# Optimization experiments

Measured on AMD Instinct MI355X. Metric: run time of the kernel, lower is better.

Reference implementation:

```python
import jax, jax.numpy as jnp
import numpy as np
import math

B, S, D, H = 2, 2048, 2048, 16
HD = D // H  # 128


def setup_inputs() -> dict:
    key = jax.random.key(0)
    ks = jax.random.split(key, 6)
    x = jax.random.normal(ks[0], (B, S, D), dtype=jnp.float32)
    scale = 1.0 / math.sqrt(D)
    wq = jax.random.normal(ks[1], (D, D), dtype=jnp.float32) * scale
    wk = jax.random.normal(ks[2], (D, D), dtype=jnp.float32) * scale
    wv = jax.random.normal(ks[3], (D, D), dtype=jnp.float32) * scale
    wo = jax.random.normal(ks[4], (D, D), dtype=jnp.float32) * scale
    # rotary frequencies: freqs_cis[t, j] = exp(i * t / theta^(2j/HD))
    theta = 10000.0
    inv = 1.0 / (theta ** (jnp.arange(0, HD, 2, dtype=jnp.float32) / HD))  # [HD//2]
    ang = jnp.arange(S, dtype=jnp.float32)[:, None] * inv[None, :]  # [S, HD//2]
    freqs_cos = jnp.cos(ang)
    freqs_sin = jnp.sin(ang)
    # causal additive mask
    mask = jnp.where(jnp.tril(jnp.ones((S, S), dtype=bool)), 0.0, -1e9)
    mask = mask[None, None, :, :].astype(jnp.float32)
    return {"x": x, "wq": wq, "wk": wk, "wv": wv, "wo": wo,
            "freqs_cos": freqs_cos, "freqs_sin": freqs_sin, "mask": mask}


def _rope(t, cos, sin):
    # t: [B, S, H, HD]; cos/sin: [S, HD//2]
    b, s, h, d = t.shape
    t2 = t.reshape(b, s, h, d // 2, 2)
    re, im = t2[..., 0], t2[..., 1]
    c = cos[None, :, None, :]
    sn = sin[None, :, None, :]
    out_re = re * c - im * sn
    out_im = re * sn + im * c
    return jnp.stack([out_re, out_im], axis=-1).reshape(b, s, h, d)


def reference(x, wq, wk, wv, wo, freqs_cos, freqs_sin, mask):
    b, s, _ = x.shape
    xq = (x @ wq.T).reshape(b, s, H, HD)
    xk = (x @ wk.T).reshape(b, s, H, HD)
    xv = (x @ wv.T).reshape(b, s, H, HD)
    xq = _rope(xq, freqs_cos, freqs_sin)
    xk = _rope(xk, freqs_cos, freqs_sin)
    # [B, H, S, HD]
    q = xq.transpose(0, 2, 1, 3)
    k = xk.transpose(0, 2, 1, 3)
    v = xv.transpose(0, 2, 1, 3)
    scores = jnp.einsum("bhqd,bhkd->bhqk", q, k) / math.sqrt(HD)
    scores = scores + mask
    probs = jax.nn.softmax(scores.astype(jnp.float32), axis=-1).astype(q.dtype)
    out = jnp.einsum("bhqk,bhkd->bhqd", probs, v)
    out = out.transpose(0, 2, 1, 3).reshape(b, s, -1)
    return out @ wo.T
```

## Files before the change

kernel.cpp:

```cpp
#include <hip/hip_runtime.h>
#include <math.h>

#define BATCH 2
#define SEQ 2048
#define DMODEL 2048
#define NH 16
#define HD 128

typedef __bf16 bf16x8 __attribute__((ext_vector_type(8)));
typedef __bf16 bf16x4 __attribute__((ext_vector_type(4)));
typedef float f32x4 __attribute__((ext_vector_type(4)));
typedef float f32x16 __attribute__((ext_vector_type(16)));

#define GLL16(dst, src)                                                          \
  __builtin_amdgcn_global_load_lds(                                              \
      (const __attribute__((address_space(1))) void*)(src),                      \
      (__attribute__((address_space(3))) void*)(dst), 16, 0, 0)

__global__ __launch_bounds__(256) void split_fp32(const float* __restrict__ src,
                                                  __bf16* __restrict__ hi,
                                                  __bf16* __restrict__ lo) {
  const size_t i = (size_t)blockIdx.x * 256 + threadIdx.x;
  const float4 v = ((const float4*)src)[i];
  bf16x4 h, L;
  h[0] = (__bf16)v.x; h[1] = (__bf16)v.y; h[2] = (__bf16)v.z; h[3] = (__bf16)v.w;
  L[0] = (__bf16)(v.x - (float)h[0]);
  L[1] = (__bf16)(v.y - (float)h[1]);
  L[2] = (__bf16)(v.z - (float)h[2]);
  L[3] = (__bf16)(v.w - (float)h[3]);
  ((bf16x4*)hi)[i] = h;
  ((bf16x4*)lo)[i] = L;
}

template <int EMIT>
__global__ __launch_bounds__(256) void gemm_bs(const __bf16* __restrict__ Ah,
                                               const __bf16* __restrict__ Al,
                                               const __bf16* __restrict__ Bh,
                                               const __bf16* __restrict__ Bl,
                                               void* __restrict__ Cout,
                                               int M, int N, int K) {
  __shared__ __bf16 sAh[4096], sAl[4096], sBh[4096], sBl[4096];
  const int tid = threadIdx.x;
  const int l = tid & 63;
  const int w = tid >> 6;
  const int lg = l >> 4, lm = l & 15;
  const int wr = w >> 1, wc = w & 1;
  const int m0 = blockIdx.y * 128, n0 = blockIdx.x * 128;

  const int sr = l >> 2;
  const int sc8 = (l & 3) * 8;
  const size_t rowA0 = (size_t)(m0 + 32 * w + sr);
  const size_t rowB0 = (size_t)(n0 + 32 * w + sr);

  f32x4 acc[4][4];
#pragma unroll
  for (int i = 0; i < 4; ++i)
#pragma unroll
    for (int j = 0; j < 4; ++j) { f32x4 z = {0.f, 0.f, 0.f, 0.f}; acc[i][j] = z; }

  for (int k0 = 0; k0 < K; k0 += 32) {
    __syncthreads();
    GLL16(sAh + 1024 * w,       Ah + rowA0 * K + k0 + sc8);
    GLL16(sAh + 1024 * w + 512, Ah + (rowA0 + 16) * K + k0 + sc8);
    GLL16(sAl + 1024 * w,       Al + rowA0 * K + k0 + sc8);
    GLL16(sAl + 1024 * w + 512, Al + (rowA0 + 16) * K + k0 + sc8);
    GLL16(sBh + 1024 * w,       Bh + rowB0 * K + k0 + sc8);
    GLL16(sBh + 1024 * w + 512, Bh + (rowB0 + 16) * K + k0 + sc8);
    GLL16(sBl + 1024 * w,       Bl + rowB0 * K + k0 + sc8);
    GLL16(sBl + 1024 * w + 512, Bl + (rowB0 + 16) * K + k0 + sc8);
    __syncthreads();

    bf16x8 fah[4], fal[4], fbh[4], fbl[4];
#pragma unroll
    for (int i = 0; i < 4; ++i) {
      const int ra = (wr * 64 + 16 * i + lm) * 32 + lg * 8;
      fah[i] = *(const bf16x8*)(sAh + ra);
      fal[i] = *(const bf16x8*)(sAl + ra);
      const int rb = (wc * 64 + 16 * i + lm) * 32 + lg * 8;
      fbh[i] = *(const bf16x8*)(sBh + rb);
      fbl[i] = *(const bf16x8*)(sBl + rb);
    }
#pragma unroll
    for (int i = 0; i < 4; ++i)
#pragma unroll
      for (int j = 0; j < 4; ++j) {
        acc[i][j] = __builtin_amdgcn_mfma_f32_16x16x32_bf16(fah[i], fbh[j], acc[i][j], 0, 0, 0);
        acc[i][j] = __builtin_amdgcn_mfma_f32_16x16x32_bf16(fah[i], fbl[j], acc[i][j], 0, 0, 0);
        acc[i][j] = __builtin_amdgcn_mfma_f32_16x16x32_bf16(fal[i], fbh[j], acc[i][j], 0, 0, 0);
      }
  }

#pragma unroll
  for (int i = 0; i < 4; ++i)
#pragma unroll
    for (int j = 0; j < 4; ++j)
#pragma unroll
      for (int r = 0; r < 4; ++r) {
        const size_t row = (size_t)(m0 + wr * 64 + 16 * i + lg * 4 + r);
        const size_t col = (size_t)(n0 + wc * 64 + 16 * j + lm);
        if (EMIT == 0) ((float*)Cout)[row * N + col] = acc[i][j][r];
        else           ((__bf16*)Cout)[row * N + col] = (__bf16)acc[i][j][r];
      }
}

__global__ __launch_bounds__(256) void rope_bf16(__bf16* __restrict__ t,
                                                 const float* __restrict__ cosp,
                                                 const float* __restrict__ sinp,
                                                 float scale) {
  const size_t i4 = (size_t)blockIdx.x * 256 + threadIdx.x;
  const size_t e = i4 * 4;
  const int srow = (int)((e >> 11) & 2047);
  const int p = (int)(e & 127) >> 1;
  bf16x4 vv = *(bf16x4*)(t + e);
  const float c0 = cosp[srow * 64 + p],     s0 = sinp[srow * 64 + p];
  const float c1 = cosp[srow * 64 + p + 1], s1 = sinp[srow * 64 + p + 1];
  const float re0 = (float)vv[0], im0 = (float)vv[1];
  const float re1 = (float)vv[2], im1 = (float)vv[3];
  bf16x4 o;
  o[0] = (__bf16)((re0 * c0 - im0 * s0) * scale);
  o[1] = (__bf16)((re0 * s0 + im0 * c0) * scale);
  o[2] = (__bf16)((re1 * c1 - im1 * s1) * scale);
  o[3] = (__bf16)((re1 * s1 + im1 * c1) * scale);
  *(bf16x4*)(t + e) = o;
}

static __device__ __forceinline__ unsigned pk2(float a, float b) {
  unsigned short x = __builtin_bit_cast(unsigned short, (__bf16)a);
  unsigned short y = __builtin_bit_cast(unsigned short, (__bf16)b);
  return ((unsigned)y << 16) | (unsigned)x;
}

__global__ __launch_bounds__(256) void attn_mfma2(const __bf16* __restrict__ q,
                                                  const __bf16* __restrict__ k,
                                                  const __bf16* __restrict__ v,
                                                  __bf16* __restrict__ oh,
                                                  __bf16* __restrict__ ol) {
  __shared__ __align__(16) char Ks[64 * 272];
  __shared__ __align__(16) char Vt[128 * 144];

  const int tid = threadIdx.x;
  const int l = tid & 63, w = tid >> 6;
  const int l31 = l & 31, hg = l >> 5;

  const int f = (int)blockIdx.x;
  const int X = f & 7, t = f >> 3;
  const int g = X * 4 + (t & 3);
  const int qt = 15 - (t >> 2);
  const int b = g >> 4, h = g & 15;
  const int q0 = qt * 128;
  const size_t bh = (size_t)b * SEQ * DMODEL + (size_t)h * HD;

  bf16x8 qf[8];
  {
    const __bf16* qr = q + bh + (size_t)(q0 + 32 * w + l31) * DMODEL;
#pragma unroll
    for (int ks = 0; ks < 8; ++ks) qf[ks] = *(const bf16x8*)(qr + ks * 16 + hg * 8);
  }

  f32x16 accO[4];
#pragma unroll
  for (int dt = 0; dt < 4; ++dt)
#pragma unroll
    for (int i = 0; i < 16; ++i) accO[dt][i] = 0.f;
  float m_own = -1e30f, l_own = 0.f;

  const int srT = tid >> 4;
  const int scT = tid & 15;
  const int nkt = 2 * qt + 2;
  const int qg_own = q0 + 32 * w + l31;
  const int qg_min = q0 + 32 * w;

  bf16x8 kst[4], vst[4];
#pragma unroll
  for (int rnd = 0; rnd < 4; ++rnd) {
    const int r = srT + 16 * rnd;
    const size_t ga = bh + (size_t)(r) * DMODEL + scT * 8;
    kst[rnd] = *(const bf16x8*)(k + ga);
    vst[rnd] = *(const bf16x8*)(v + ga);
  }

  for (int kt = 0; kt < nkt; ++kt) {
    const int k0 = kt * 64;
    __syncthreads();
#pragma unroll
    for (int rnd = 0; rnd < 4; ++rnd) {
      const int r = srT + 16 * rnd;
      *(bf16x8*)(Ks + r * 272 + ((scT * 16) ^ (((r >> 3) & 7) << 4))) = kst[rnd];
      const int swz = (scT & 7) << 4;
      const int cb = (2 * r) ^ swz;
#pragma unroll
      for (int e = 0; e < 8; ++e)
        *(__bf16*)(Vt + (scT * 8 + e) * 144 + cb) = vst[rnd][e];
    }
    __syncthreads();
    if (kt + 1 < nkt) {
#pragma unroll
      for (int rnd = 0; rnd < 4; ++rnd) {
        const int r = srT + 16 * rnd;
        const size_t ga = bh + (size_t)((kt + 1) * 64 + r) * DMODEL + scT * 8;
        kst[rnd] = *(const bf16x8*)(k + ga);
        vst[rnd] = *(const bf16x8*)(v + ga);
      }
    }
    if (k0 > qg_min + 31) continue;

    f32x16 sc[2];
#pragma unroll
    for (int mt = 0; mt < 2; ++mt)
#pragma unroll
      for (int i = 0; i < 16; ++i) sc[mt][i] = 0.f;
#pragma unroll
    for (int mt = 0; mt < 2; ++mt) {
      const int row = mt * 32 + l31;
      const char* kr = Ks + row * 272;
      const int sx = ((row >> 3) & 7) << 4;
#pragma unroll
      for (int ks = 0; ks < 8; ++ks) {
        bf16x8 kf = *(const bf16x8*)(kr + ((ks * 32 + hg * 16) ^ sx));
        sc[mt] = __builtin_amdgcn_mfma_f32_32x32x16_bf16(kf, qf[ks], sc[mt], 0, 0, 0);
      }
    }

    if (k0 + 63 > qg_min) {
#pragma unroll
      for (int mt = 0; mt < 2; ++mt)
#pragma unroll
        for (int ri = 0; ri < 16; ++ri) {
          const int kg = k0 + mt * 32 + (ri & 3) + 8 * (ri >> 2) + 4 * hg;
          if (kg > qg_own) sc[mt][ri] = -INFINITY;
        }
    }

    float tm = -INFINITY;
#pragma unroll
    for (int mt = 0; mt < 2; ++mt)
#pragma unroll
      for (int ri = 0; ri < 16; ++ri) tm = fmaxf(tm, sc[mt][ri]);
    tm = fmaxf(tm, __shfl_xor(tm, 32));

    if (__any(tm > m_own)) {
      const float mnew = fmaxf(m_own, tm);
      const float alpha = __expf(m_own - mnew);
      m_own = mnew;
      l_own *= alpha;
#pragma unroll
      for (int ri = 0; ri < 16; ++ri) {
        const float a = __shfl(alpha, (ri & 3) + 8 * (ri >> 2) + 4 * hg);
#pragma unroll
        for (int dt = 0; dt < 4; ++dt) accO[dt][ri] *= a;
      }
    }
    float rs = 0.f;
#pragma unroll
    for (int mt = 0; mt < 2; ++mt)
#pragma unroll
      for (int ri = 0; ri < 16; ++ri) {
        const float p = __expf(sc[mt][ri] - m_own);
        sc[mt][ri] = p;
        rs += p;
      }
    rs += __shfl_xor(rs, 32);
    l_own += rs;

#pragma unroll
    for (int kk = 0; kk < 4; ++kk) {
      const int mt = kk >> 1, J8 = (kk & 1) * 8;
      unsigned oL0 = pk2(sc[mt][J8 + 0], sc[mt][J8 + 1]);
      unsigned oL1 = pk2(sc[mt][J8 + 2], sc[mt][J8 + 3]);
      unsigned oH0 = pk2(sc[mt][J8 + 4], sc[mt][J8 + 5]);
      unsigned oH1 = pk2(sc[mt][J8 + 6], sc[mt][J8 + 7]);
      unsigned s0 = hg ? oL0 : oH0;
      unsigned s1 = hg ? oL1 : oH1;
      const unsigned r0 = (unsigned)__shfl_xor((int)s0, 32);
      const unsigned r1 = (unsigned)__shfl_xor((int)s1, 32);
      int4 fi;
      fi.x = (int)(hg ? r0 : oL0);
      fi.y = (int)(hg ? r1 : oL1);
      fi.z = (int)(hg ? oH0 : r0);
      fi.w = (int)(hg ? oH1 : r1);
      const bf16x8 pa = __builtin_bit_cast(bf16x8, fi);
      const int kb = (kk * 32 + hg * 16);
#pragma unroll
      for (int dt = 0; dt < 4; ++dt) {
        const int d = dt * 32 + l31;
        bf16x8 vf = *(const bf16x8*)(Vt + d * 144 + (kb ^ (((d >> 3) & 7) << 4)));
        accO[dt] = __builtin_amdgcn_mfma_f32_32x32x16_bf16(pa, vf, accO[dt], 0, 0, 0);
      }
    }
  }

  const float inv_own = 1.f / l_own;
#pragma unroll
  for (int ri = 0; ri < 16; ++ri) {
    const int row = (ri & 3) + 8 * (ri >> 2) + 4 * hg;
    const float il = __shfl(inv_own, row & 31);
    const size_t rbase = bh + (size_t)(q0 + 32 * w + row) * DMODEL;
#pragma unroll
    for (int dt = 0; dt < 4; ++dt) {
      const float val = accO[dt][ri] * il;
      const size_t idx = rbase + dt * 32 + l31;
      const __bf16 hv = (__bf16)val;
      oh[idx] = hv;
      ol[idx] = (__bf16)(val - (float)hv);
    }
  }
}

extern "C" void kernel_launch(void* const* d_in, const int* in_sizes, int n_in,
                              void* d_out, int out_size, void* d_ws, size_t ws_size,
                              hipStream_t stream) {
  const float* x  = (const float*)d_in[0];
  const float* wq = (const float*)d_in[1];
  const float* wk = (const float*)d_in[2];
  const float* wv = (const float*)d_in[3];
  const float* wo = (const float*)d_in[4];
  const float* fc = (const float*)d_in[5];
  const float* fs = (const float*)d_in[6];

  const size_t NTOK = (size_t)BATCH * SEQ;
  const size_t NE   = NTOK * DMODEL;

  char* wsb = (char*)d_ws;
  __bf16* xh = (__bf16*)wsb;
  __bf16* xl = xh + NE;
  __bf16* wh = (__bf16*)(wsb + 2 * NE * 2);
  __bf16* wl = wh + (size_t)DMODEL * DMODEL;
  __bf16* vb = (__bf16*)(wsb + 2 * NE * 2 + 2 * (size_t)DMODEL * DMODEL * 2);
  __bf16* oh = xh;
  __bf16* ol = xl;
  __bf16* qb = (__bf16*)d_out;
  __bf16* kb = qb + NE;

  const dim3 gg(DMODEL / 128, (unsigned)(NTOK / 128));
  const int sx = (int)(NE / 4 / 256);
  const int sw = DMODEL * DMODEL / 4 / 256;

  split_fp32<<<sx, 256, 0, stream>>>(x, xh, xl);

  split_fp32<<<sw, 256, 0, stream>>>(wq, wh, wl);
  gemm_bs<1><<<gg, 256, 0, stream>>>(xh, xl, wh, wl, qb, (int)NTOK, DMODEL, DMODEL);
  split_fp32<<<sw, 256, 0, stream>>>(wk, wh, wl);
  gemm_bs<1><<<gg, 256, 0, stream>>>(xh, xl, wh, wl, kb, (int)NTOK, DMODEL, DMODEL);
  split_fp32<<<sw, 256, 0, stream>>>(wv, wh, wl);
  gemm_bs<1><<<gg, 256, 0, stream>>>(xh, xl, wh, wl, vb, (int)NTOK, DMODEL, DMODEL);

  rope_bf16<<<sx, 256, 0, stream>>>(qb, fc, fs, 0.08838834764831845f);
  rope_bf16<<<sx, 256, 0, stream>>>(kb, fc, fs, 1.0f);

  attn_mfma2<<<dim3(512), 256, 0, stream>>>(qb, kb, vb, oh, ol);

  split_fp32<<<sw, 256, 0, stream>>>(wo, wh, wl);
  gemm_bs<0><<<gg, 256, 0, stream>>>(oh, ol, wh, wl, (float*)d_out, (int)NTOK, DMODEL, DMODEL);
}
```

Baseline: 670.0 us.

## Replace split-bf16 GEMM with pipelined 256x128 tile kernel and swizzled LDS

The old 128x128 GEMM did synchronous global-to-LDS loads each K step, with a barrier before and after. It is replaced by a 512-thread kernel with 256x128 tiles, triple-buffered A and double-buffered B in swizzled LDS, and loads issued asynchronously ahead of the MFMAs. The three hi/lo partial products are folded into one 96-step K loop over concatenated segments. The kernel also uses a fixed block-to-tile mapping, s_setprio around MFMA bursts and manual vmcnt waits. The aim is to hide memory latency and cut LDS bank conflicts. The trade-offs are 128 KB of dynamic LDS, hardcoded problem sizes and fragile hand-written wait counts.

Result: no change. 673.4 us (+0.5%).

```diff
diff --git a/kernel.cpp b/kernel.cpp
--- a/kernel.cpp
+++ b/kernel.cpp
@@ -33,24 +33,55 @@
 }
 
 template <int EMIT>
-__global__ __launch_bounds__(256) void gemm_bs(const __bf16* __restrict__ Ah,
-                                               const __bf16* __restrict__ Al,
-                                               const __bf16* __restrict__ Bh,
-                                               const __bf16* __restrict__ Bl,
-                                               void* __restrict__ Cout,
-                                               int M, int N, int K) {
-  __shared__ __bf16 sAh[4096], sAl[4096], sBh[4096], sBl[4096];
+__global__ __launch_bounds__(512, 2) void gemm8(const __bf16* __restrict__ Ah,
+                                                const __bf16* __restrict__ Al,
+                                                const __bf16* __restrict__ Bh,
+                                                const __bf16* __restrict__ Bl,
+                                                void* __restrict__ Cout) {
+  extern __shared__ char sm[];
+  constexpr int NT = 96;
   const int tid = threadIdx.x;
-  const int l = tid & 63;
-  const int w = tid >> 6;
+  const int l = tid & 63, w = tid >> 6;
   const int lg = l >> 4, lm = l & 15;
   const int wr = w >> 1, wc = w & 1;
-  const int m0 = blockIdx.y * 128, n0 = blockIdx.x * 128;
-
-  const int sr = l >> 2;
-  const int sc8 = (l & 3) * 8;
-  const size_t rowA0 = (size_t)(m0 + 32 * w + sr);
-  const size_t rowB0 = (size_t)(n0 + 32 * w + sr);
+
+  const int bid = (int)blockIdx.x;
+  const int X = bid & 7, sub = bid >> 3;
+  const int mb = (X & 3) * 4 + (sub >> 3);
+  const int nb = (X >> 2) * 8 + (sub & 7);
+  const int m0 = mb * 256, n0 = nb * 128;
+
+  const __bf16* segA[3] = {Ah, Al, Ah};
+  const __bf16* segB[3] = {Bh, Bh, Bl};
+
+  const int srow = l >> 3;
+  const int co = ((l & 7) ^ srow) * 8;
+
+  char* const Abuf = sm;
+  char* const Bbuf = sm + 98304;
+
+  auto stageB = [&](int tb) {
+    char* bd = Bbuf + (tb & 1) * 16384;
+    const __bf16* sb = segB[tb >> 5];
+    const int kw = (tb & 31) * 64;
+#pragma unroll
+    for (int j = 0; j < 2; ++j)
+      GLL16(bd + (w * 2 + j) * 1024,
+            sb + (size_t)(n0 + (w * 2 + j) * 8 + srow) * 2048 + kw + co);
+  };
+  auto stageAu = [&](int ta, int slot, int u) {
+    char* ad = Abuf + slot * 32768 + u * 16384;
+    const __bf16* sa = segA[ta >> 5];
+    const int kw = (ta & 31) * 64;
+#pragma unroll
+    for (int j = 0; j < 2; ++j)
+      GLL16(ad + (w * 2 + j) * 1024,
+            sa + (size_t)(m0 + u * 128 + (w * 2 + j) * 8 + srow) * 2048 + kw + co);
+  };
+
+  stageAu(0, 0, 0); stageAu(0, 0, 1);
+  stageB(0);
+  stageAu(1, 1, 0); stageAu(1, 1, 1);
 
   f32x4 acc[4][4];
 #pragma unroll
@@ -58,36 +89,79 @@
 #pragma unroll
     for (int j = 0; j < 4; ++j) { f32x4 z = {0.f, 0.f, 0.f, 0.f}; acc[i][j] = z; }
 
-  for (int k0 = 0; k0 < K; k0 += 32) {
-    __syncthreads();
-    GLL16(sAh + 1024 * w,       Ah + rowA0 * K + k0 + sc8);
-    GLL16(sAh + 1024 * w + 512, Ah + (rowA0 + 16) * K + k0 + sc8);
-    GLL16(sAl + 1024 * w,       Al + rowA0 * K + k0 + sc8);
-    GLL16(sAl + 1024 * w + 512, Al + (rowA0 + 16) * K + k0 + sc8);
-    GLL16(sBh + 1024 * w,       Bh + rowB0 * K + k0 + sc8);
-    GLL16(sBh + 1024 * w + 512, Bh + (rowB0 + 16) * K + k0 + sc8);
-    GLL16(sBl + 1024 * w,       Bl + rowB0 * K + k0 + sc8);
-    GLL16(sBl + 1024 * w + 512, Bl + (rowB0 + 16) * K + k0 + sc8);
-    __syncthreads();
-
-    bf16x8 fah[4], fal[4], fbh[4], fbl[4];
-#pragma unroll
-    for (int i = 0; i < 4; ++i) {
-      const int ra = (wr * 64 + 16 * i + lm) * 32 + lg * 8;
-      fah[i] = *(const bf16x8*)(sAh + ra);
-      fal[i] = *(const bf16x8*)(sAl + ra);
-      const int rb = (wc * 64 + 16 * i + lm) * 32 + lg * 8;
-      fbh[i] = *(const bf16x8*)(sBh + rb);
-      fbl[i] = *(const bf16x8*)(sBl + rb);
-    }
-#pragma unroll
-    for (int i = 0; i < 4; ++i)
-#pragma unroll
-      for (int j = 0; j < 4; ++j) {
-        acc[i][j] = __builtin_amdgcn_mfma_f32_16x16x32_bf16(fah[i], fbh[j], acc[i][j], 0, 0, 0);
-        acc[i][j] = __builtin_amdgcn_mfma_f32_16x16x32_bf16(fah[i], fbl[j], acc[i][j], 0, 0, 0);
-        acc[i][j] = __builtin_amdgcn_mfma_f32_16x16x32_bf16(fal[i], fbh[j], acc[i][j], 0, 0, 0);
-      }
+  int sA = 0, sA2 = 2;
+  const int swz = lm & 7;
+
+  for (int t = 0; t < NT; ++t) {
+    if (t + 1 < NT) { asm volatile("s_waitcnt vmcnt(4)" ::: "memory"); }
+    else            { asm volatile("s_waitcnt vmcnt(0)" ::: "memory"); }
+    __builtin_amdgcn_sched_barrier(0);
+    __builtin_amdgcn_s_barrier();
+
+    const char* Ab = Abuf + sA * 32768;
+    const char* Bb = Bbuf + (t & 1) * 16384;
+
+    bf16x8 b0[4], b1[4], a[2];
+
+    if (t + 1 < NT) stageB(t + 1);
+#pragma unroll
+    for (int j = 0; j < 4; ++j)
+      b0[j] = *(const bf16x8*)(Bb + (wc * 64 + j * 16 + lm) * 128 + ((lg ^ swz) << 4));
+#pragma unroll
+    for (int i = 0; i < 2; ++i)
+      a[i] = *(const bf16x8*)(Ab + (wr * 64 + i * 16 + lm) * 128 + ((lg ^ swz) << 4));
+    __builtin_amdgcn_s_barrier();
+    __builtin_amdgcn_s_setprio(1);
+#pragma unroll
+    for (int i = 0; i < 2; ++i)
+#pragma unroll
+      for (int j = 0; j < 4; ++j)
+        acc[i][j] = __builtin_amdgcn_mfma_f32_16x16x32_bf16(a[i], b0[j], acc[i][j], 0, 0, 0);
+    __builtin_amdgcn_s_setprio(0);
+
+    if (t + 2 < NT) stageAu(t + 2, sA2, 0);
+#pragma unroll
+    for (int j = 0; j < 4; ++j)
+      b1[j] = *(const bf16x8*)(Bb + (wc * 64 + j * 16 + lm) * 128 + (((4 + lg) ^ swz) << 4));
+#pragma unroll
+    for (int i = 0; i < 2; ++i)
+      a[i] = *(const bf16x8*)(Ab + (wr * 64 + i * 16 + lm) * 128 + (((4 + lg) ^ swz) << 4));
+    __builtin_amdgcn_s_barrier();
+    __builtin_amdgcn_s_setprio(1);
+#pragma unroll
+    for (int i = 0; i < 2; ++i)
+#pragma unroll
+      for (int j = 0; j < 4; ++j)
+        acc[i][j] = __builtin_amdgcn_mfma_f32_16x16x32_bf16(a[i], b1[j], acc[i][j], 0, 0, 0);
+    __builtin_amdgcn_s_setprio(0);
+
+    if (t + 2 < NT) stageAu(t + 2, sA2, 1);
+#pragma unroll
+    for (int i = 0; i < 2; ++i)
+      a[i] = *(const bf16x8*)(Ab + (wr * 64 + (2 + i) * 16 + lm) * 128 + ((lg ^ swz) << 4));
+    __builtin_amdgcn_s_barrier();
+    __builtin_amdgcn_s_setprio(1);
+#pragma unroll
+    for (int i = 0; i < 2; ++i)
+#pragma unroll
+      for (int j = 0; j < 4; ++j)
+        acc[2 + i][j] = __builtin_amdgcn_mfma_f32_16x16x32_bf16(a[i], b0[j], acc[2 + i][j], 0, 0, 0);
+    __builtin_amdgcn_s_setprio(0);
+
+#pragma unroll
+    for (int i = 0; i < 2; ++i)
+      a[i] = *(const bf16x8*)(Ab + (wr * 64 + (2 + i) * 16 + lm) * 128 + (((4 + lg) ^ swz) << 4));
+    __builtin_amdgcn_s_barrier();
+    __builtin_amdgcn_s_setprio(1);
+#pragma unroll
+    for (int i = 0; i < 2; ++i)
+#pragma unroll
+      for (int j = 0; j < 4; ++j)
+        acc[2 + i][j] = __builtin_amdgcn_mfma_f32_16x16x32_bf16(a[i], b1[j], acc[2 + i][j], 0, 0, 0);
+    __builtin_amdgcn_s_setprio(0);
+
+    sA = (sA == 2) ? 0 : sA + 1;
+    sA2 = (sA2 == 2) ? 0 : sA2 + 1;
   }
 
 #pragma unroll
@@ -96,10 +170,10 @@
     for (int j = 0; j < 4; ++j)
 #pragma unroll
       for (int r = 0; r < 4; ++r) {
-        const size_t row = (size_t)(m0 + wr * 64 + 16 * i + lg * 4 + r);
-        const size_t col = (size_t)(n0 + wc * 64 + 16 * j + lm);
-        if (EMIT == 0) ((float*)Cout)[row * N + col] = acc[i][j][r];
-        else           ((__bf16*)Cout)[row * N + col] = (__bf16)acc[i][j][r];
+        const size_t row = (size_t)(m0 + wr * 64 + i * 16 + lg * 4 + r);
+        const size_t col = (size_t)(n0 + wc * 64 + j * 16 + lm);
+        if (EMIT == 0) ((float*)Cout)[row * 2048 + col] = acc[i][j][r];
+        else           ((__bf16*)Cout)[row * 2048 + col] = (__bf16)acc[i][j][r];
       }
 }
 
@@ -331,18 +405,23 @@
   __bf16* qb = (__bf16*)d_out;
   __bf16* kb = qb + NE;
 
-  const dim3 gg(DMODEL / 128, (unsigned)(NTOK / 128));
   const int sx = (int)(NE / 4 / 256);
   const int sw = DMODEL * DMODEL / 4 / 256;
+  const int SMEM = 131072;
+
+  (void)hipFuncSetAttribute((const void*)gemm8<1>,
+                            hipFuncAttributeMaxDynamicSharedMemorySize, SMEM);
+  (void)hipFuncSetAttribute((const void*)gemm8<0>,
+                            hipFuncAttributeMaxDynamicSharedMemorySize, SMEM);
 
   split_fp32<<<sx, 256, 0, stream>>>(x, xh, xl);
 
   split_fp32<<<sw, 256, 0, stream>>>(wq, wh, wl);
-  gemm_bs<1><<<gg, 256, 0, stream>>>(xh, xl, wh, wl, qb, (int)NTOK, DMODEL, DMODEL);
+  gemm8<1><<<256, 512, SMEM, stream>>>(xh, xl, wh, wl, qb);
   split_fp32<<<sw, 256, 0, stream>>>(wk, wh, wl);
-  gemm_bs<1><<<gg, 256, 0, stream>>>(xh, xl, wh, wl, kb, (int)NTOK, DMODEL, DMODEL);
+  gemm8<1><<<256, 512, SMEM, stream>>>(xh, xl, wh, wl, kb);
   split_fp32<<<sw, 256, 0, stream>>>(wv, wh, wl);
-  gemm_bs<1><<<gg, 256, 0, stream>>>(xh, xl, wh, wl, vb, (int)NTOK, DMODEL, DMODEL);
+  gemm8<1><<<256, 512, SMEM, stream>>>(xh, xl, wh, wl, vb);
 
   rope_bf16<<<sx, 256, 0, stream>>>(qb, fc, fs, 0.08838834764831845f);
   rope_bf16<<<sx, 256, 0, stream>>>(kb, fc, fs, 1.0f);
@@ -350,5 +429,5 @@
   attn_mfma2<<<dim3(512), 256, 0, stream>>>(qb, kb, vb, oh, ol);
 
   split_fp32<<<sw, 256, 0, stream>>>(wo, wh, wl);
-  gemm_bs<0><<<gg, 256, 0, stream>>>(oh, ol, wh, wl, (float*)d_out, (int)NTOK, DMODEL, DMODEL);
-}
+  gemm8<0><<<256, 512, SMEM, stream>>>(oh, ol, wh, wl, (float*)d_out);
+}
```
